# Kernel tuning notes

Hardware: AMD Instinct MI355X
Metric: run time of the kernel (lower is better)

Reference implementation:

```python
import jax, jax.numpy as jnp
from jax import lax
import numpy as np

DC = 3.79
HSTEP = 0.1
EPS = 1e-5
BIG = 1e10

def conv1(x, K):
    p = (K.shape[-1] - 1) // 2
    return lax.conv_general_dilated(x, K, (1,), [(p, p)], dimension_numbers=("NCH", "OIH", "NCH"))

def conv1T(x, K):
    # conv_transpose1d(stride=1, padding=p) == conv1d with flipped kernel and swapped in/out channels
    return conv1(x, jnp.flip(jnp.swapaxes(K, 0, 1), -1))

def masked_instance_norm(x, mask, eps=EPS):
    denom = jnp.sum(mask, axis=2, keepdims=True)
    mean = jnp.sum(x * mask, axis=2, keepdims=True) / denom
    meanm = mean * mask  # original multiplies the broadcast mean by the mask
    var = jnp.sum(((x - meanm) * mask) ** 2, axis=2, keepdims=True) / denom
    return (x - meanm) / jnp.sqrt(var + eps)

def avg_pool3s2(x):
    # torch avg_pool1d(kernel=3, stride=2, padding=1, count_include_pad=True)
    s = lax.reduce_window(x, 0.0, lax.add, (1, 1, 3), (1, 1, 2), [(0, 0), (0, 0), (1, 1)])
    return s / 3.0

def dist_constraint(X, M_fixed, M_padding, dc=DC):
    # X: [nb,3,n]; M_fixed, M_padding: [nb,1,n]. Vectorized (scan) version of the
    # original per-segment python loops: left/right propagation from fixed anchors
    # via unit-step (length dc) cumulative sums, blended by distance weights.
    dX = X[:, :, 1:] - X[:, :, :-1]
    d = jnp.sum(dX * dX, axis=1, keepdims=True)  # [nb,1,n-1]
    avM = jnp.floor((M_padding[..., 1:] + M_padding[..., :-1]) / 2.0) < 0.5
    dXn = dX / jnp.sqrt(d + avM) * jnp.where(avM, 0.0, dc)  # [nb,3,n-1]
    fixed = M_fixed[:, 0, :] == 1  # [nb,n]

    Xt = jnp.moveaxis(X, 2, 0)      # [n,nb,3]
    dXnt = jnp.moveaxis(dXn, 2, 0)  # [n-1,nb,3]
    ft = fixed.T                    # [n,nb]

    def lstep(carry, inp):
        prev, seen, wl = carry
        xj, dxn, fj = inp
        val = jnp.where(fj[:, None] | ~seen[:, None], xj, prev + dxn)
        wl2 = (wl + 1.0) * (~fj)
        return (val, seen | fj, wl2), (val, wl2)

    wl0 = jnp.where(ft[0], 0.0, BIG)
    _, (lv, lw) = lax.scan(lstep, (Xt[0], ft[0], wl0), (Xt[1:], dXnt, ft[1:]))
    Xleft = jnp.concatenate([X[:, :, :1], jnp.moveaxis(lv, 0, 2)], axis=2)
    wl = jnp.concatenate([wl0[:, None], lw.T], axis=1)  # [nb,n]

    def rstep(carry, inp):
        nxt, seen, wr = carry
        xj, dxn, fj = inp
        val = jnp.where(fj[:, None] | ~seen[:, None], xj, nxt - dxn)
        wr2 = (wr + 1.0) * (~fj)
        return (val, seen | fj, wr2), (val, wr2)

    wrN = jnp.where(ft[-1], 0.0, BIG)
    _, (rv, rw) = lax.scan(rstep, (Xt[-1], ft[-1], wrN), (Xt[:-1], dXnt, ft[:-1]), reverse=True)
    Xright = jnp.concatenate([jnp.moveaxis(rv, 0, 2), X[:, :, -1:]], axis=2)
    wr = jnp.concatenate([rw.T, wrN[:, None]], axis=1)

    ws = wl + wr
    ws_safe = jnp.where(ws == 0.0, 1.0, ws)
    cl = jnp.where(ws == 0.0, 0.5, wr / ws_safe)  # weight on Xleft = (wsum-wl)/wsum
    cr = jnp.where(ws == 0.0, 0.5, wl / ws_safe)
    X2 = Xleft * cl[:, None, :] + Xright * cr[:, None, :]
    return X2 * M_padding

def tr2dist(Y):
    # pairwise Euclidean distances from coords [nb,3,n] -> [nb,n,n]
    Z = jnp.swapaxes(Y, 1, 2)
    Z = Z - jnp.mean(Z, axis=1, keepdims=True)
    sq = jnp.sum(Z * Z, axis=2)
    D2 = sq[:, :, None] + sq[:, None, :] - 2.0 * jnp.einsum("bic,bjc->bij", Z, Z)
    return jnp.sqrt(jnp.maximum(D2, 0.0) + 1e-8)

def vnet_forward(x, mask, Ks, W):
    coords = x[:, -4:-1, :]
    mask_coords = jnp.repeat((x[:, -1, :] == 1)[:, None, :], 3, axis=1)
    m = mask[:, None, :]
    nL = len(Ks)
    xc = jax.nn.relu(masked_instance_norm(conv1(x, Ks[0]) * m, m))  # dropout_p=0 -> identity
    xS, mS = [], []
    for i in range(1, nL):
        K = Ks[i]
        if K.shape[0] == K.shape[1]:
            z = jax.nn.relu(masked_instance_norm(conv1(xc, K) * m, m))
            xc = xc - HSTEP * (conv1T(z, K) * m)
        else:
            xS.append(xc)
            xc = jax.nn.relu(masked_instance_norm(conv1(xc, K) * m, m))
            mS.append(m)
            m = (avg_pool3s2(m) >= 0.5).astype(x.dtype)
            xc = avg_pool3s2(xc) * m
    ns = len(xS)
    for i in reversed(range(1, nL)):
        K = Ks[i]
        if K.shape[0] == K.shape[1]:
            z = jax.nn.relu(masked_instance_norm(conv1T(xc, K) * m, m))
            xc = xc - HSTEP * (conv1(z, K) * m)
        else:
            ns -= 1
            m = mS[ns]
            xc = jnp.repeat(xc, 2, axis=-1) * m  # F.interpolate(scale=2, mode='nearest')
            z = masked_instance_norm(conv1T(xc, K) * m, m)
            xc = jax.nn.relu(z) + xS[ns]
    xc = conv1(xc, W) * m
    xc = jnp.where(mask_coords, coords, xc)
    xout = dist_constraint(xc, mask_coords[:, :1, :].astype(x.dtype), m)
    return tr2dist(xout), xout

def setup_inputs() -> dict:
    key = jax.random.key(0)
    ks = jax.random.split(key, 12)
    nb, n = 8, 2048
    feats = jax.random.normal(ks[0], (nb, 20, n), dtype=jnp.float32)
    coords = jax.random.normal(ks[1], (nb, 3, n), dtype=jnp.float32)
    lengths = jax.random.randint(ks[2], (nb,), n // 2, n + 1)
    mask = (jnp.arange(n)[None, :] < lengths[:, None]).astype(jnp.float32)  # ragged padding mask
    flag = (jax.random.uniform(ks[3], (nb, n)) < 0.5).astype(jnp.float32) * mask  # fixed-coord flag
    x = jnp.concatenate([feats, coords, flag[:, None, :]], axis=1)

    def unif(k, shape, stdv):
        return jax.random.uniform(k, shape, jnp.float32, -stdv, stdv)

    K0 = unif(ks[4], (32, 24, 3), 0.1 * 24 / 32)
    K1 = unif(ks[5], (32, 32, 3), 0.01)
    K2 = unif(ks[6], (32, 32, 3), 0.01)
    K3 = unif(ks[7], (64, 32, 3), 0.1 * 32 / 64)
    K4 = unif(ks[8], (64, 64, 3), 0.01)
    K5 = unif(ks[9], (64, 64, 3), 0.01)
    K6 = unif(ks[10], (128, 64, 3), 0.1 * 64 / 128)
    W = 0.1 * jax.random.normal(ks[11], (3, 32, 1), dtype=jnp.float32)
    return {"x": x, "mask": mask, "K0": K0, "K1": K1, "K2": K2, "K3": K3, "K4": K4, "K5": K5, "K6": K6, "W": W}

def reference(x, mask, K0, K1, K2, K3, K4, K5, K6, W):
    dists, xout = vnet_forward(x, mask, [K0, K1, K2, K3, K4, K5, K6], W)
    return (dists, xout)
```

## Files before the change

### kernel.cpp

```cpp
#include <hip/hip_runtime.h>
#include <math.h>

#define HSTEP 0.1f
#define EPS_IN 1e-5f
#define BIGF 1e10f
#define DCF 3.79f

typedef float v4f __attribute__((ext_vector_type(4)));

__device__ inline float block_sum1(float v, float* sred) {
    #pragma unroll
    for (int off = 32; off > 0; off >>= 1) v += __shfl_down(v, off);
    int wid = threadIdx.x >> 6;
    int nw  = blockDim.x >> 6;
    if ((threadIdx.x & 63) == 0) sred[wid] = v;
    __syncthreads();
    float total = 0.f;
    for (int i = 0; i < nw; ++i) total += sred[i];
    __syncthreads();
    return total;
}

__device__ inline float2 block_sum2(float a, float b, float2* sred) {
    #pragma unroll
    for (int off = 32; off > 0; off >>= 1) {
        a += __shfl_down(a, off);
        b += __shfl_down(b, off);
    }
    int wid = threadIdx.x >> 6;
    int nw  = blockDim.x >> 6;
    if ((threadIdx.x & 63) == 0) sred[wid] = make_float2(a, b);
    __syncthreads();
    float ta = 0.f, tb = 0.f;
    for (int i = 0; i < nw; ++i) { ta += sred[i].x; tb += sred[i].y; }
    __syncthreads();
    return make_float2(ta, tb);
}

template<int CIN, bool TR>
__global__ void __launch_bounds__(1024)
conv_in_relu_kernel(const float* __restrict__ xin, float* __restrict__ out,
                    const float* __restrict__ K, int Cout, int N,
                    const float* __restrict__ mask, const float* __restrict__ denom,
                    const float* __restrict__ skip)
{
    __shared__ float srow[2048];
    __shared__ float swt[CIN * 3];
    __shared__ float2 sred[16];

    const int b   = blockIdx.x / Cout;
    const int co  = blockIdx.x % Cout;
    const int tid = threadIdx.x;

    for (int i = tid; i < CIN * 3; i += blockDim.x) {
        int ci = i / 3, k = i % 3;
        swt[i] = TR ? K[((size_t)ci * Cout + co) * 3 + (2 - k)]
                    : K[((size_t)co * CIN + ci) * 3 + k];
    }
    __syncthreads();

    const float* mrow = mask + (size_t)b * N;
    const float* xb   = xin + (size_t)b * CIN * N;
    float lsum = 0.f, lss = 0.f;
    for (int n = tid; n < N; n += 1024) {
        float acc = 0.f;
        const float* xr = xb + n;
        #pragma unroll 8
        for (int ci = 0; ci < CIN; ++ci, xr += N) {
            float xm = (n > 0)     ? xr[-1] : 0.f;
            float x0 = xr[0];
            float xp = (n < N - 1) ? xr[1]  : 0.f;
            acc = fmaf(swt[ci * 3 + 0], xm, acc);
            acc = fmaf(swt[ci * 3 + 1], x0, acc);
            acc = fmaf(swt[ci * 3 + 2], xp, acc);
        }
        float v = acc * mrow[n];
        srow[n] = v;
        lsum += v;
        lss  += v * v;
    }
    float dn = denom[b];
    float2 s = block_sum2(lsum, lss, sred);
    float mean = s.x / dn;
    float var  = s.y / dn - mean * mean;
    float inv  = 1.f / sqrtf(var + EPS_IN);

    float* orow = out + ((size_t)b * Cout + co) * N;
    const float* skrow = skip ? skip + ((size_t)b * Cout + co) * N : nullptr;
    for (int n = tid; n < N; n += 1024) {
        float mk = mrow[n];
        float zv = (srow[n] - mean * mk) * inv;
        float r  = fmaxf(zv, 0.f);
        if (skrow) r += skrow[n];
        orow[n] = r;
    }
}

template<int CIN, bool TR>
__global__ void __launch_bounds__(1024)
conv_axpy_kernel(const float* __restrict__ z, float* __restrict__ xc,
                 const float* __restrict__ K, int Cout, int N,
                 const float* __restrict__ mask)
{
    __shared__ float swt[CIN * 3];
    const int b   = blockIdx.x / Cout;
    const int co  = blockIdx.x % Cout;
    const int tid = threadIdx.x;

    for (int i = tid; i < CIN * 3; i += blockDim.x) {
        int ci = i / 3, k = i % 3;
        swt[i] = TR ? K[((size_t)ci * Cout + co) * 3 + (2 - k)]
                    : K[((size_t)co * CIN + ci) * 3 + k];
    }
    __syncthreads();

    const float* mrow = mask + (size_t)b * N;
    const float* zb   = z + (size_t)b * CIN * N;
    float* orow = xc + ((size_t)b * Cout + co) * N;
    for (int n = tid; n < N; n += 1024) {
        float acc = 0.f;
        const float* zr = zb + n;
        #pragma unroll 8
        for (int ci = 0; ci < CIN; ++ci, zr += N) {
            float xm = (n > 0)     ? zr[-1] : 0.f;
            float x0 = zr[0];
            float xp = (n < N - 1) ? zr[1]  : 0.f;
            acc = fmaf(swt[ci * 3 + 0], xm, acc);
            acc = fmaf(swt[ci * 3 + 1], x0, acc);
            acc = fmaf(swt[ci * 3 + 2], xp, acc);
        }
        orow[n] -= HSTEP * acc * mrow[n];
    }
}

__global__ void __launch_bounds__(256)
mask_prep_kernel(const float* __restrict__ mask, float* __restrict__ M1,
                 float* __restrict__ M2, float* __restrict__ d0, float* __restrict__ d1)
{
    __shared__ float sm1[1024];
    __shared__ float sredf[4];
    int b = blockIdx.x, tid = threadIdx.x;
    const float* mr = mask + (size_t)b * 2048;

    float s0 = 0.f;
    for (int n = tid; n < 2048; n += 256) s0 += mr[n];
    float t0 = block_sum1(s0, sredf);
    if (tid == 0) d0[b] = t0;

    for (int n = tid; n < 1024; n += 256) {
        float s = mr[2 * n];
        if (2 * n - 1 >= 0)   s += mr[2 * n - 1];
        if (2 * n + 1 < 2048) s += mr[2 * n + 1];
        float v = (s * (1.f / 3.f) >= 0.5f) ? 1.f : 0.f;
        sm1[n] = v;
        M1[(size_t)b * 1024 + n] = v;
    }
    __syncthreads();
    float s1 = 0.f;
    for (int n = tid; n < 1024; n += 256) s1 += sm1[n];
    float t1 = block_sum1(s1, sredf);
    if (tid == 0) d1[b] = t1;

    for (int n = tid; n < 512; n += 256) {
        float s = sm1[2 * n];
        if (2 * n - 1 >= 0)   s += sm1[2 * n - 1];
        if (2 * n + 1 < 1024) s += sm1[2 * n + 1];
        M2[(size_t)b * 512 + n] = (s * (1.f / 3.f) >= 0.5f) ? 1.f : 0.f;
    }
}

__global__ void pool_x_kernel(const float* __restrict__ xin, float* __restrict__ xout,
                              const float* __restrict__ mnew, int C, int Nin, int Nout, int B)
{
    int idx = blockIdx.x * blockDim.x + threadIdx.x;
    if (idx >= B * C * Nout) return;
    int n  = idx % Nout;
    int bc = idx / Nout;
    int b  = bc / C;
    const float* r = xin + (size_t)bc * Nin;
    float s = r[2 * n];
    if (2 * n - 1 >= 0)  s += r[2 * n - 1];
    if (2 * n + 1 < Nin) s += r[2 * n + 1];
    xout[idx] = s * (1.f / 3.f) * mnew[(size_t)b * Nout + n];
}

__global__ void upsample_kernel(const float* __restrict__ xin, float* __restrict__ xout,
                                const float* __restrict__ mask, int C, int Nout, int B)
{
    int idx = blockIdx.x * blockDim.x + threadIdx.x;
    if (idx >= B * C * Nout) return;
    int n  = idx % Nout;
    int bc = idx / Nout;
    int b  = bc / C;
    xout[idx] = xin[(size_t)bc * (Nout / 2) + (n >> 1)] * mask[(size_t)b * Nout + n];
}

__global__ void __launch_bounds__(1024)
dc_all_kernel(const float* __restrict__ xc32, const float* __restrict__ x,
              const float* __restrict__ W, const float* __restrict__ mask,
              const float* __restrict__ den, float* __restrict__ xout, int N)
{
    __shared__ float sX[3][2048];
    __shared__ float sD[3][2048];
    __shared__ float sM[2048];
    __shared__ unsigned long long smk[32];
    __shared__ float sW[96];

    const int b = blockIdx.x, tid = threadIdx.x;
    if (tid < 96) sW[tid] = W[tid];
    __syncthreads();

    const float* xb      = xc32 + (size_t)b * 32 * N;
    const float* flagrow = x + ((size_t)b * 24 + 23) * N;

    #pragma unroll
    for (int r = 0; r < 2; ++r) {
        int n = tid + r * 1024;
        float mk = mask[(size_t)b * N + n];
        float fl = flagrow[n];
        float v0 = 0.f, v1 = 0.f, v2 = 0.f;
        #pragma unroll 8
        for (int ci = 0; ci < 32; ++ci) {
            float xv = xb[(size_t)ci * N + n];
            v0 = fmaf(sW[0 * 32 + ci], xv, v0);
            v1 = fmaf(sW[1 * 32 + ci], xv, v1);
            v2 = fmaf(sW[2 * 32 + ci], xv, v2);
        }
        v0 *= mk; v1 *= mk; v2 *= mk;
        bool fixed = (fl == 1.f);
        if (fixed) {
            v0 = x[((size_t)b * 24 + 20) * N + n];
            v1 = x[((size_t)b * 24 + 21) * N + n];
            v2 = x[((size_t)b * 24 + 22) * N + n];
        }
        sX[0][n] = v0; sX[1][n] = v1; sX[2][n] = v2; sM[n] = mk;
        unsigned long long bm = __ballot(fixed);
        if ((tid & 63) == 0) smk[n >> 6] = bm;
    }
    __syncthreads();

    #pragma unroll
    for (int r = 0; r < 2; ++r) {
        int n = tid + r * 1024;
        if (n < N - 1) {
            float d0 = sX[0][n + 1] - sX[0][n];
            float d1 = sX[1][n + 1] - sX[1][n];
            float d2 = sX[2][n + 1] - sX[2][n];
            float d  = d0 * d0 + d1 * d1 + d2 * d2;
            bool avM = floorf((sM[n] + sM[n + 1]) * 0.5f) < 0.5f;
            if (avM) {
                sD[0][n] = 0.f; sD[1][n] = 0.f; sD[2][n] = 0.f;
            } else {
                float sq = sqrtf(d);
                sD[0][n] = (d0 / sq) * DCF;
                sD[1][n] = (d1 / sq) * DCF;
                sD[2][n] = (d2 / sq) * DCF;
            }
        }
    }
    __syncthreads();

    int len = (int)den[b];

    #pragma unroll
    for (int r = 0; r < 2; ++r) {
        int j  = tid + r * 1024;
        int cc = j >> 6, jl = j & 63;

        unsigned long long below = smk[cc] & (~0ull >> (63 - jl));
        int p = -1;
        if (below) p = (cc << 6) + 63 - __clzll(below);
        else {
            for (int c2 = cc - 1; c2 >= 0; --c2) {
                unsigned long long m = smk[c2];
                if (m) { p = (c2 << 6) + 63 - __clzll(m); break; }
            }
        }
        float l0, l1, l2, wl;
        if (p >= 0) {
            wl = (float)(j - p);
            l0 = sX[0][p]; l1 = sX[1][p]; l2 = sX[2][p];
            int kend = min(j, len - 1);
            for (int k = p; k < kend; ++k) {
                l0 += sD[0][k]; l1 += sD[1][k]; l2 += sD[2][k];
            }
        } else { wl = BIGF; l0 = sX[0][j]; l1 = sX[1][j]; l2 = sX[2][j]; }

        unsigned long long above = smk[cc] & (~0ull << jl);
        int q = -1;
        if (above) q = (cc << 6) + __ffsll(above) - 1;
        else {
            for (int c2 = cc + 1; c2 < 32; ++c2) {
                unsigned long long m = smk[c2];
                if (m) { q = (c2 << 6) + __ffsll(m) - 1; break; }
            }
        }
        float r0, r1, r2, wr;
        if (q >= 0) {
            wr = (float)(q - j);
            r0 = sX[0][q]; r1 = sX[1][q]; r2 = sX[2][q];
            for (int k = q - 1; k >= j; --k) {
                r0 -= sD[0][k]; r1 -= sD[1][k]; r2 -= sD[2][k];
            }
        } else { wr = BIGF; r0 = sX[0][j]; r1 = sX[1][j]; r2 = sX[2][j]; }

        float ws_ = wl + wr, cl, cr;
        if (ws_ == 0.f) { cl = 0.5f; cr = 0.5f; }
        else            { cl = wr / ws_; cr = wl / ws_; }
        float mk = sM[j];
        xout[((size_t)b * 3 + 0) * N + j] = (l0 * cl + r0 * cr) * mk;
        xout[((size_t)b * 3 + 1) * N + j] = (l1 * cl + r1 * cr) * mk;
        xout[((size_t)b * 3 + 2) * N + j] = (l2 * cl + r2 * cr) * mk;
    }
}

__global__ void __launch_bounds__(256)
tr2dist_kernel(const float* __restrict__ Y, float* __restrict__ out)
{
    const int b    = blockIdx.x >> 8;
    const int tile = blockIdx.x & 255;
    const int tid  = threadIdx.x;
    const float* yb = Y + (size_t)b * 6144;

    const int jA = tid * 4;
    const int jB = 1024 + tid * 4;
    const float4 cA0 = *(const float4*)(yb + jA);
    const float4 cA1 = *(const float4*)(yb + 2048 + jA);
    const float4 cA2 = *(const float4*)(yb + 4096 + jA);
    const float4 cB0 = *(const float4*)(yb + jB);
    const float4 cB1 = *(const float4*)(yb + 2048 + jB);
    const float4 cB2 = *(const float4*)(yb + 4096 + jB);

    #pragma unroll
    for (int r = 0; r < 8; ++r) {
        const int i = tile * 8 + r;
        const float y0 = yb[i], y1 = yb[2048 + i], y2 = yb[4096 + i];
        v4f oA, oB;
        {
            float d0 = y0 - cA0.x, d1 = y1 - cA1.x, d2 = y2 - cA2.x;
            oA.x = sqrtf(fmaf(d0, d0, fmaf(d1, d1, fmaf(d2, d2, 1e-8f))));
            d0 = y0 - cA0.y; d1 = y1 - cA1.y; d2 = y2 - cA2.y;
            oA.y = sqrtf(fmaf(d0, d0, fmaf(d1, d1, fmaf(d2, d2, 1e-8f))));
            d0 = y0 - cA0.z; d1 = y1 - cA1.z; d2 = y2 - cA2.z;
            oA.z = sqrtf(fmaf(d0, d0, fmaf(d1, d1, fmaf(d2, d2, 1e-8f))));
            d0 = y0 - cA0.w; d1 = y1 - cA1.w; d2 = y2 - cA2.w;
            oA.w = sqrtf(fmaf(d0, d0, fmaf(d1, d1, fmaf(d2, d2, 1e-8f))));
        }
        {
            float d0 = y0 - cB0.x, d1 = y1 - cB1.x, d2 = y2 - cB2.x;
            oB.x = sqrtf(fmaf(d0, d0, fmaf(d1, d1, fmaf(d2, d2, 1e-8f))));
            d0 = y0 - cB0.y; d1 = y1 - cB1.y; d2 = y2 - cB2.y;
            oB.y = sqrtf(fmaf(d0, d0, fmaf(d1, d1, fmaf(d2, d2, 1e-8f))));
            d0 = y0 - cB0.z; d1 = y1 - cB1.z; d2 = y2 - cB2.z;
            oB.z = sqrtf(fmaf(d0, d0, fmaf(d1, d1, fmaf(d2, d2, 1e-8f))));
            d0 = y0 - cB0.w; d1 = y1 - cB1.w; d2 = y2 - cB2.w;
            oB.w = sqrtf(fmaf(d0, d0, fmaf(d1, d1, fmaf(d2, d2, 1e-8f))));
        }
        float* orow = out + ((size_t)b * 2048 + i) * 2048;
        __builtin_nontemporal_store(oA, (v4f*)(orow + jA));
        __builtin_nontemporal_store(oB, (v4f*)(orow + jB));
    }
}

extern "C" void kernel_launch(void* const* d_in, const int* in_sizes, int n_in,
                              void* d_out, int out_size, void* d_ws, size_t ws_size,
                              hipStream_t stream)
{
    const float* x    = (const float*)d_in[0];
    const float* mask = (const float*)d_in[1];
    const float* K0   = (const float*)d_in[2];
    const float* K1   = (const float*)d_in[3];
    const float* K2   = (const float*)d_in[4];
    const float* K3   = (const float*)d_in[5];
    const float* K4   = (const float*)d_in[6];
    const float* K5   = (const float*)d_in[7];
    const float* K6   = (const float*)d_in[8];
    const float* W    = (const float*)d_in[9];
    float* out = (float*)d_out;
    float* ws  = (float*)d_ws;
    (void)in_sizes; (void)n_in; (void)out_size; (void)ws_size;

    const int B = 8, N = 2048;
    size_t off = 0;
    auto alloc = [&](size_t nf) { float* p = ws + off; off += nf; return p; };

    float* M1   = alloc((size_t)B * 1024);
    float* M2   = alloc((size_t)B * 512);
    float* DEN0 = alloc(8);
    float* DEN1 = alloc(8);
    float* BUF0 = alloc(1048576);
    float* BUF1 = alloc(1048576);
    float* BUF2 = alloc(1048576);
    float* BUF3 = alloc(1048576);

    auto cdiv = [](int a, int b_) { return (a + b_ - 1) / b_; };
    float* XOUT = out + (size_t)B * N * N;

    mask_prep_kernel<<<8, 256, 0, stream>>>(mask, M1, M2, DEN0, DEN1);

    conv_in_relu_kernel<24, false><<<B * 32, 1024, 0, stream>>>(x, BUF0, K0, 32, 2048, mask, DEN0, nullptr);

    conv_in_relu_kernel<32, false><<<B * 32, 1024, 0, stream>>>(BUF0, BUF1, K1, 32, 2048, mask, DEN0, nullptr);
    conv_axpy_kernel<32, true><<<B * 32, 1024, 0, stream>>>(BUF1, BUF0, K1, 32, 2048, mask);
    conv_in_relu_kernel<32, false><<<B * 32, 1024, 0, stream>>>(BUF0, BUF1, K2, 32, 2048, mask, DEN0, nullptr);
    conv_axpy_kernel<32, true><<<B * 32, 1024, 0, stream>>>(BUF1, BUF0, K2, 32, 2048, mask);

    conv_in_relu_kernel<32, false><<<B * 64, 1024, 0, stream>>>(BUF0, BUF1, K3, 64, 2048, mask, DEN0, nullptr);
    pool_x_kernel<<<cdiv(B * 64 * 1024, 256), 256, 0, stream>>>(BUF1, BUF2, M1, 64, 2048, 1024, B);

    conv_in_relu_kernel<64, false><<<B * 64, 1024, 0, stream>>>(BUF2, BUF1, K4, 64, 1024, M1, DEN1, nullptr);
    conv_axpy_kernel<64, true><<<B * 64, 1024, 0, stream>>>(BUF1, BUF2, K4, 64, 1024, M1);
    conv_in_relu_kernel<64, false><<<B * 64, 1024, 0, stream>>>(BUF2, BUF1, K5, 64, 1024, M1, DEN1, nullptr);
    conv_axpy_kernel<64, true><<<B * 64, 1024, 0, stream>>>(BUF1, BUF2, K5, 64, 1024, M1);

    conv_in_relu_kernel<64, false><<<B * 128, 1024, 0, stream>>>(BUF2, BUF1, K6, 128, 1024, M1, DEN1, nullptr);
    pool_x_kernel<<<cdiv(B * 128 * 512, 256), 256, 0, stream>>>(BUF1, BUF3, M2, 128, 1024, 512, B);

    upsample_kernel<<<cdiv(B * 128 * 1024, 256), 256, 0, stream>>>(BUF3, BUF1, M1, 128, 1024, B);
    conv_in_relu_kernel<128, true><<<B * 64, 1024, 0, stream>>>(BUF1, BUF3, K6, 64, 1024, M1, DEN1, BUF2);

    conv_in_relu_kernel<64, true><<<B * 64, 1024, 0, stream>>>(BUF3, BUF1, K5, 64, 1024, M1, DEN1, nullptr);
    conv_axpy_kernel<64, false><<<B * 64, 1024, 0, stream>>>(BUF1, BUF3, K5, 64, 1024, M1);
    conv_in_relu_kernel<64, true><<<B * 64, 1024, 0, stream>>>(BUF3, BUF1, K4, 64, 1024, M1, DEN1, nullptr);
    conv_axpy_kernel<64, false><<<B * 64, 1024, 0, stream>>>(BUF1, BUF3, K4, 64, 1024, M1);

    upsample_kernel<<<cdiv(B * 64 * 2048, 256), 256, 0, stream>>>(BUF3, BUF1, mask, 64, 2048, B);
    conv_in_relu_kernel<64, true><<<B * 32, 1024, 0, stream>>>(BUF1, BUF2, K3, 32, 2048, mask, DEN0, BUF0);

    conv_in_relu_kernel<32, true><<<B * 32, 1024, 0, stream>>>(BUF2, BUF1, K2, 32, 2048, mask, DEN0, nullptr);
    conv_axpy_kernel<32, false><<<B * 32, 1024, 0, stream>>>(BUF1, BUF2, K2, 32, 2048, mask);
    conv_in_relu_kernel<32, true><<<B * 32, 1024, 0, stream>>>(BUF2, BUF1, K1, 32, 2048, mask, DEN0, nullptr);
    conv_axpy_kernel<32, false><<<B * 32, 1024, 0, stream>>>(BUF1, BUF2, K1, 32, 2048, mask);

    dc_all_kernel<<<8, 1024, 0, stream>>>(BUF2, x, W, mask, DEN0, XOUT, N);

    tr2dist_kernel<<<8 * 256, 256, 0, stream>>>(XOUT, out);
}
```

Baseline: 443.0 us.

## Fuse avg-pool and nearest upsample into conv+instance-norm kernels

```diff
diff --git a/kernel.cpp b/kernel.cpp
--- a/kernel.cpp
+++ b/kernel.cpp
@@ -37,12 +37,13 @@
     return make_float2(ta, tb);
 }
 
-template<int CIN, bool TR>
+template<int CIN, bool TR, bool UPS, bool POOL>
 __global__ void __launch_bounds__(1024)
 conv_in_relu_kernel(const float* __restrict__ xin, float* __restrict__ out,
                     const float* __restrict__ K, int Cout, int N,
                     const float* __restrict__ mask, const float* __restrict__ denom,
-                    const float* __restrict__ skip)
+                    const float* __restrict__ skip, float* __restrict__ pool,
+                    const float* __restrict__ mhalf)
 {
     __shared__ float srow[2048];
     __shared__ float swt[CIN * 3];
@@ -59,17 +60,25 @@
     }
     __syncthreads();
 
+    const int srcw = UPS ? (N >> 1) : N;
     const float* mrow = mask + (size_t)b * N;
-    const float* xb   = xin + (size_t)b * CIN * N;
+    const float* xb   = xin + (size_t)b * CIN * srcw;
     float lsum = 0.f, lss = 0.f;
     for (int n = tid; n < N; n += 1024) {
         float acc = 0.f;
-        const float* xr = xb + n;
         #pragma unroll 8
-        for (int ci = 0; ci < CIN; ++ci, xr += N) {
-            float xm = (n > 0)     ? xr[-1] : 0.f;
-            float x0 = xr[0];
-            float xp = (n < N - 1) ? xr[1]  : 0.f;
+        for (int ci = 0; ci < CIN; ++ci) {
+            const float* src = xb + (size_t)ci * srcw;
+            float xm, x0, xp;
+            if (!UPS) {
+                xm = (n > 0)     ? src[n - 1] : 0.f;
+                x0 = src[n];
+                xp = (n < N - 1) ? src[n + 1] : 0.f;
+            } else {
+                x0 = src[n >> 1] * mrow[n];
+                xm = (n > 0)     ? src[(n - 1) >> 1] * mrow[n - 1] : 0.f;
+                xp = (n < N - 1) ? src[(n + 1) >> 1] * mrow[n + 1] : 0.f;
+            }
             acc = fmaf(swt[ci * 3 + 0], xm, acc);
             acc = fmaf(swt[ci * 3 + 1], x0, acc);
             acc = fmaf(swt[ci * 3 + 2], xp, acc);
@@ -85,14 +94,25 @@
     float var  = s.y / dn - mean * mean;
     float inv  = 1.f / sqrtf(var + EPS_IN);
 
-    float* orow = out + ((size_t)b * Cout + co) * N;
+    float* orow = POOL ? nullptr : out + ((size_t)b * Cout + co) * N;
     const float* skrow = skip ? skip + ((size_t)b * Cout + co) * N : nullptr;
     for (int n = tid; n < N; n += 1024) {
         float mk = mrow[n];
         float zv = (srow[n] - mean * mk) * inv;
         float r  = fmaxf(zv, 0.f);
         if (skrow) r += skrow[n];
-        orow[n] = r;
+        if (POOL) srow[n] = r;
+        else      orow[n] = r;
+    }
+    if (POOL) {
+        __syncthreads();
+        const int Nh = N >> 1;
+        const float* mh = mhalf + (size_t)b * Nh;
+        float* prow = pool + ((size_t)b * Cout + co) * Nh;
+        for (int np = tid; np < Nh; np += 1024) {
+            float zm1 = (np > 0) ? srow[2 * np - 1] : 0.f;
+            prow[np] = (zm1 + srow[2 * np] + srow[2 * np + 1]) * (1.f / 3.f) * mh[np];
+        }
     }
 }
 
@@ -167,32 +187,6 @@
         if (2 * n + 1 < 1024) s += sm1[2 * n + 1];
         M2[(size_t)b * 512 + n] = (s * (1.f / 3.f) >= 0.5f) ? 1.f : 0.f;
     }
-}
-
-__global__ void pool_x_kernel(const float* __restrict__ xin, float* __restrict__ xout,
-                              const float* __restrict__ mnew, int C, int Nin, int Nout, int B)
-{
-    int idx = blockIdx.x * blockDim.x + threadIdx.x;
-    if (idx >= B * C * Nout) return;
-    int n  = idx % Nout;
-    int bc = idx / Nout;
-    int b  = bc / C;
-    const float* r = xin + (size_t)bc * Nin;
-    float s = r[2 * n];
-    if (2 * n - 1 >= 0)  s += r[2 * n - 1];
-    if (2 * n + 1 < Nin) s += r[2 * n + 1];
-    xout[idx] = s * (1.f / 3.f) * mnew[(size_t)b * Nout + n];
-}
-
-__global__ void upsample_kernel(const float* __restrict__ xin, float* __restrict__ xout,
-                                const float* __restrict__ mask, int C, int Nout, int B)
-{
-    int idx = blockIdx.x * blockDim.x + threadIdx.x;
-    if (idx >= B * C * Nout) return;
-    int n  = idx % Nout;
-    int bc = idx / Nout;
-    int b  = bc / C;
-    xout[idx] = xin[(size_t)bc * (Nout / 2) + (n >> 1)] * mask[(size_t)b * Nout + n];
 }
 
 __global__ void __launch_bounds__(1024)
@@ -393,43 +387,39 @@
     float* BUF2 = alloc(1048576);
     float* BUF3 = alloc(1048576);
 
-    auto cdiv = [](int a, int b_) { return (a + b_ - 1) / b_; };
     float* XOUT = out + (size_t)B * N * N;
+    float* NUL  = nullptr;
 
     mask_prep_kernel<<<8, 256, 0, stream>>>(mask, M1, M2, DEN0, DEN1);
 
-    conv_in_relu_kernel<24, false><<<B * 32, 1024, 0, stream>>>(x, BUF0, K0, 32, 2048, mask, DEN0, nullptr);
-
-    conv_in_relu_kernel<32, false><<<B * 32, 1024, 0, stream>>>(BUF0, BUF1, K1, 32, 2048, mask, DEN0, nullptr);
+    conv_in_relu_kernel<24, false, false, false><<<B * 32, 1024, 0, stream>>>(x, BUF0, K0, 32, 2048, mask, DEN0, NUL, NUL, NUL);
+
+    conv_in_relu_kernel<32, false, false, false><<<B * 32, 1024, 0, stream>>>(BUF0, BUF1, K1, 32, 2048, mask, DEN0, NUL, NUL, NUL);
     conv_axpy_kernel<32, true><<<B * 32, 1024, 0, stream>>>(BUF1, BUF0, K1, 32, 2048, mask);
-    conv_in_relu_kernel<32, false><<<B * 32, 1024, 0, stream>>>(BUF0, BUF1, K2, 32, 2048, mask, DEN0, nullptr);
+    conv_in_relu_kernel<32, false, false, false><<<B * 32, 1024, 0, stream>>>(BUF0, BUF1, K2, 32, 2048, mask, DEN0, NUL, NUL, NUL);
     conv_axpy_kernel<32, true><<<B * 32, 1024, 0, stream>>>(BUF1, BUF0, K2, 32, 2048, mask);
 
-    conv_in_relu_kernel<32, false><<<B * 64, 1024, 0, stream>>>(BUF0, BUF1, K3, 64, 2048, mask, DEN0, nullptr);
-    pool_x_kernel<<<cdiv(B * 64 * 1024, 256), 256, 0, stream>>>(BUF1, BUF2, M1, 64, 2048, 1024, B);
-
-    conv_in_relu_kernel<64, false><<<B * 64, 1024, 0, stream>>>(BUF2, BUF1, K4, 64, 1024, M1, DEN1, nullptr);
+    conv_in_relu_kernel<32, false, false, true><<<B * 64, 1024, 0, stream>>>(BUF0, NUL, K3, 64, 2048, mask, DEN0, NUL, BUF2, M1);
+
+    conv_in_relu_kernel<64, false, false, false><<<B * 64, 1024, 0, stream>>>(BUF2, BUF1, K4, 64, 1024, M1, DEN1, NUL, NUL, NUL);
     conv_axpy_kernel<64, true><<<B * 64, 1024, 0, stream>>>(BUF1, BUF2, K4, 64, 1024, M1);
-    conv_in_relu_kernel<64, false><<<B * 64, 1024, 0, stream>>>(BUF2, BUF1, K5, 64, 1024, M1, DEN1, nullptr);
+    conv_in_relu_kernel<64, false, false, false><<<B * 64, 1024, 0, stream>>>(BUF2, BUF1, K5, 64, 1024, M1, DEN1, NUL, NUL, NUL);
     conv_axpy_kernel<64, true><<<B * 64, 1024, 0, stream>>>(BUF1, BUF2, K5, 64, 1024, M1);
 
-    conv_in_relu_kernel<64, false><<<B * 128, 1024, 0, stream>>>(BUF2, BUF1, K6, 128, 1024, M1, DEN1, nullptr);
-    pool_x_kernel<<<cdiv(B * 128 * 512, 256), 256, 0, stream>>>(BUF1, BUF3, M2, 128, 1024, 512, B);
-
-    upsample_kernel<<<cdiv(B * 128 * 1024, 256), 256, 0, stream>>>(BUF3, BUF1, M1, 128, 1024, B);
-    conv_in_relu_kernel<128, true><<<B * 64, 1024, 0, stream>>>(BUF1, BUF3, K6, 64, 1024, M1, DEN1, BUF2);
-
-    conv_in_relu_kernel<64, true><<<B * 64, 1024, 0, stream>>>(BUF3, BUF1, K5, 64, 1024, M1, DEN1, nullptr);
-    conv_axpy_kernel<64, false><<<B * 64, 1024, 0, stream>>>(BUF1, BUF3, K5, 64, 1024, M1);
-    conv_in_relu_kernel<64, true><<<B * 64, 1024, 0, stream>>>(BUF3, BUF1, K4, 64, 1024, M1, DEN1, nullptr);
-    conv_axpy_kernel<64, false><<<B * 64, 1024, 0, stream>>>(BUF1, BUF3, K4, 64, 1024, M1);
-
-    upsample_kernel<<<cdiv(B * 64 * 2048, 256), 256, 0, stream>>>(BUF3, BUF1, mask, 64, 2048, B);
-    conv_in_relu_kernel<64, true><<<B * 32, 1024, 0, stream>>>(BUF1, BUF2, K3, 32, 2048, mask, DEN0, BUF0);
-
-    conv_in_relu_kernel<32, true><<<B * 32, 1024, 0, stream>>>(BUF2, BUF1, K2, 32, 2048, mask, DEN0, nullptr);
+    conv_in_relu_kernel<64, false, false, true><<<B * 128, 1024, 0, stream>>>(BUF2, NUL, K6, 128, 1024, M1, DEN1, NUL, BUF3, M2);
+
+    conv_in_relu_kernel<128, true, true, false><<<B * 64, 1024, 0, stream>>>(BUF3, BUF1, K6, 64, 1024, M1, DEN1, BUF2, NUL, NUL);
+
+    conv_in_relu_kernel<64, true, false, false><<<B * 64, 1024, 0, stream>>>(BUF1, BUF2, K5, 64, 1024, M1, DEN1, NUL, NUL, NUL);
+    conv_axpy_kernel<64, false><<<B * 64, 1024, 0, stream>>>(BUF2, BUF1, K5, 64, 1024, M1);
+    conv_in_relu_kernel<64, true, false, false><<<B * 64, 1024, 0, stream>>>(BUF1, BUF2, K4, 64, 1024, M1, DEN1, NUL, NUL, NUL);
+    conv_axpy_kernel<64, false><<<B * 64, 1024, 0, stream>>>(BUF2, BUF1, K4, 64, 1024, M1);
+
+    conv_in_relu_kernel<64, true, true, false><<<B * 32, 1024, 0, stream>>>(BUF1, BUF2, K3, 32, 2048, mask, DEN0, BUF0, NUL, NUL);
+
+    conv_in_relu_kernel<32, true, false, false><<<B * 32, 1024, 0, stream>>>(BUF2, BUF1, K2, 32, 2048, mask, DEN0, NUL, NUL, NUL);
     conv_axpy_kernel<32, false><<<B * 32, 1024, 0, stream>>>(BUF1, BUF2, K2, 32, 2048, mask);
-    conv_in_relu_kernel<32, true><<<B * 32, 1024, 0, stream>>>(BUF2, BUF1, K1, 32, 2048, mask, DEN0, nullptr);
+    conv_in_relu_kernel<32, true, false, false><<<B * 32, 1024, 0, stream>>>(BUF2, BUF1, K1, 32, 2048, mask, DEN0, NUL, NUL, NUL);
     conv_axpy_kernel<32, false><<<B * 32, 1024, 0, stream>>>(BUF1, BUF2, K1, 32, 2048, mask);
 
     dc_all_kernel<<<8, 1024, 0, stream>>>(BUF2, x, W, mask, DEN0, XOUT, N);
```

Result: slower. 543.5 us (+22.7%).
